# Kernel optimization log

Measured on AMD Instinct MI355X. Metric: run time of the kernel, lower is better.

## Reference

```python
import jax, jax.numpy as jnp
import numpy as np
import math

B, S, D = 8, 4096, 128  # batch, seq_len, embed_dim == attention_head_size
EPS = 1e-5


def layer_norm(x, w, b):
    mu = jnp.mean(x, axis=-1, keepdims=True)
    var = jnp.var(x, axis=-1, keepdims=True)
    return (x - mu) * jax.lax.rsqrt(var + EPS) * w + b


def setup_inputs() -> dict:
    key = jax.random.key(0)
    ks = jax.random.split(key, 4)
    x = jax.random.normal(ks[0], (B, S, D), dtype=jnp.float32)
    Wq = jax.random.normal(ks[1], (D, D), dtype=jnp.float32) / math.sqrt(D)
    Wk = jax.random.normal(ks[2], (D, D), dtype=jnp.float32) / math.sqrt(D)
    Wv = jax.random.normal(ks[3], (D, D), dtype=jnp.float32) / math.sqrt(D)
    qn_w = jnp.ones((D,), dtype=jnp.float32)
    qn_b = jnp.zeros((D,), dtype=jnp.float32)
    kn_w = jnp.ones((D,), dtype=jnp.float32)
    kn_b = jnp.zeros((D,), dtype=jnp.float32)
    return {"x": x, "Wq": Wq, "Wk": Wk, "Wv": Wv,
            "qn_w": qn_w, "qn_b": qn_b, "kn_w": kn_w, "kn_b": kn_b}


def reference(x, Wq, Wk, Wv, qn_w, qn_b, kn_w, kn_b):
    # q/k/v projections (nn.Linear with no bias: x @ W^T)
    q = layer_norm(jnp.einsum('bsd,hd->bsh', x, Wq), qn_w, qn_b)
    k = layer_norm(jnp.einsum('bsd,hd->bsh', x, Wk), kn_w, kn_b)
    v = jnp.einsum('bsd,hd->bsh', x, Wv)
    scale = math.sqrt(D)
    scores = jnp.einsum('bqh,bkh->bqk', q, k) / scale  # [B, S, S]
    attn = jax.nn.softmax(scores, axis=-1)
    # dropout_rate = 0.0 -> identity
    return jnp.einsum('bqk,bkh->bqh', attn, v)
```

## Files before the change

kernel.cpp:

```cpp
#include <hip/hip_runtime.h>

#define B_ 8
#define S_ 4096
#define D_ 128
#define KVB 64
#define NT (S_ / KVB)

typedef __attribute__((ext_vector_type(4))) float f32x4;
typedef __attribute__((ext_vector_type(16))) float f32x16;
typedef __attribute__((ext_vector_type(8))) short s16x8;

__device__ __forceinline__ unsigned short f2bf(float f) {
    union { float f; unsigned u; } v; v.f = f;
    unsigned r = (v.u + 0x7fffu + ((v.u >> 16) & 1u)) >> 16;
    return (unsigned short)r;
}

__device__ __forceinline__ unsigned cvt_pk(float lo, float hi) {
    unsigned r;
    asm("v_cvt_pk_bf16_f32 %0, %1, %2" : "=v"(r) : "v"(lo), "v"(hi));
    return r;
}

__device__ __forceinline__ s16x8 load_cvt8(const float* p) {
    f32x4 a = *(const f32x4*)p;
    f32x4 b = *(const f32x4*)(p + 4);
    s16x8 r;
    r[0] = (short)f2bf(a[0]); r[1] = (short)f2bf(a[1]);
    r[2] = (short)f2bf(a[2]); r[3] = (short)f2bf(a[3]);
    r[4] = (short)f2bf(b[0]); r[5] = (short)f2bf(b[1]);
    r[6] = (short)f2bf(b[2]); r[7] = (short)f2bf(b[3]);
    return r;
}

__device__ __forceinline__ void gld16(unsigned short* lds, const unsigned short* g) {
    __builtin_amdgcn_global_load_lds(
        (const __attribute__((address_space(1))) unsigned int*)g,
        (__attribute__((address_space(3))) unsigned int*)lds,
        16, 0, 0);
}

__global__ __launch_bounds__(256, 1) void proj_kernel(
    const float* __restrict__ x,  const float* __restrict__ Wq,
    const float* __restrict__ Wk, const float* __restrict__ Wv,
    const float* __restrict__ qn_w, const float* __restrict__ qn_b,
    const float* __restrict__ kn_w, const float* __restrict__ kn_b,
    unsigned short* __restrict__ qo, unsigned short* __restrict__ ko,
    unsigned short* __restrict__ vto)
{
    __shared__ unsigned short wlds[128 * 136];
    __shared__ unsigned short vstage[128 * 72];

    const int tid  = threadIdx.x;
    const int lane = tid & 63;
    const int wv   = tid >> 6;
    const int j    = lane & 15;
    const int g    = lane >> 4;

    const int b    = blockIdx.x >> 6;
    const int sblk = (blockIdx.x & 63) * 64;
    const int srow = sblk + wv * 16;

    const float* xrow = x + ((size_t)b * S_ + srow + j) * D_;
    s16x8 af[4];
#pragma unroll
    for (int kk = 0; kk < 4; ++kk) af[kk] = load_cvt8(xrow + kk * 32 + g * 8);

    const int wrow = tid >> 1;
    const int wcol = (tid & 1) * 64;

#pragma unroll 1
    for (int m = 0; m < 3; ++m) {
        const float* Wm = (m == 0) ? Wq : (m == 1) ? Wk : Wv;
        __syncthreads();
#pragma unroll
        for (int it = 0; it < 8; ++it) {
            int col = wcol + it * 8;
            *(s16x8*)&wlds[wrow * 136 + col] = load_cvt8(Wm + wrow * 128 + col);
        }
        __syncthreads();

        f32x4 acc[8];
#pragma unroll
        for (int ct = 0; ct < 8; ++ct) { f32x4 z = {0.f, 0.f, 0.f, 0.f}; acc[ct] = z; }
#pragma unroll
        for (int ct = 0; ct < 8; ++ct) {
#pragma unroll
            for (int kk = 0; kk < 4; ++kk) {
                s16x8 bf = *(const s16x8*)&wlds[(ct * 16 + j) * 136 + kk * 32 + g * 8];
                acc[ct] = __builtin_amdgcn_mfma_f32_16x16x32_bf16(af[kk], bf, acc[ct], 0, 0, 0);
            }
        }

        if (m < 2) {
            const float* lw = (m == 0) ? qn_w : kn_w;
            const float* lb = (m == 0) ? qn_b : kn_b;
            float sum[4], sq[4];
#pragma unroll
            for (int r = 0; r < 4; ++r) {
                float s1 = 0.f, s2 = 0.f;
#pragma unroll
                for (int ct = 0; ct < 8; ++ct) { float v = acc[ct][r]; s1 += v; s2 += v * v; }
#pragma unroll
                for (int msk = 1; msk < 16; msk <<= 1) {
                    s1 += __shfl_xor(s1, msk);
                    s2 += __shfl_xor(s2, msk);
                }
                sum[r] = s1; sq[r] = s2;
            }
            float gwv[8], gbv[8];
#pragma unroll
            for (int ct = 0; ct < 8; ++ct) { gwv[ct] = lw[ct * 16 + j]; gbv[ct] = lb[ct * 16 + j]; }
            unsigned short* dst = (m == 0) ? qo : ko;
            const float post = (m == 0) ? 0.12751742361888f : 1.0f;
#pragma unroll
            for (int r = 0; r < 4; ++r) {
                float mean = sum[r] * (1.f / 128.f);
                float var  = sq[r] * (1.f / 128.f) - mean * mean;
                float rstd = rsqrtf(var + 1e-5f);
                size_t rowoff = ((size_t)b * S_ + sblk + wv * 16 + g * 4 + r) * D_;
#pragma unroll
                for (int ct = 0; ct < 8; ++ct) {
                    float val = ((acc[ct][r] - mean) * rstd * gwv[ct] + gbv[ct]) * post;
                    dst[rowoff + ct * 16 + j] = f2bf(val);
                }
            }
        } else {
#pragma unroll
            for (int ct = 0; ct < 8; ++ct) {
#pragma unroll
                for (int r = 0; r < 4; ++r) {
                    vstage[(ct * 16 + j) * 72 + wv * 16 + g * 4 + r] = f2bf(acc[ct][r]);
                }
            }
            __syncthreads();
            int h  = tid >> 1;
            int cb = (tid & 1) * 32;
#pragma unroll
            for (int c = 0; c < 4; ++c) {
                *(s16x8*)(vto + ((size_t)b * D_ + h) * S_ + sblk + cb + c * 8) =
                    *(const s16x8*)&vstage[h * 72 + cb + c * 8];
            }
        }
    }
}

__global__ __launch_bounds__(256, 2) void attn_kernel(
    const unsigned short* __restrict__ qb, const unsigned short* __restrict__ kb,
    const unsigned short* __restrict__ vtb, float* __restrict__ out)
{
    __shared__ unsigned short kbuf[2][KVB * D_];
    __shared__ unsigned short vbuf[2][D_ * KVB];

    const int tid  = threadIdx.x;
    const int lane = tid & 63;
    const int wv   = tid >> 6;
    const int qg   = wv & 1;
    const int kh   = wv >> 1;
    const int a    = lane & 31;
    const int hh   = lane >> 5;

    const int blk = (a >> 2) & 3;
    const int pa  = (blk == 1) ? a + 4 : (blk == 2) ? a - 4 : a;

    const int swz = (blockIdx.x & 7) * 64 + (blockIdx.x >> 3);
    const int b   = swz >> 6;
    const int s0  = (swz & 63) * 64;

    const unsigned short* qptr = qb + ((size_t)b * S_ + s0 + qg * 32 + a) * D_;
    s16x8 qf[8];
#pragma unroll
    for (int kk = 0; kk < 8; ++kk) qf[kk] = *(const s16x8*)(qptr + kk * 16 + hh * 8);

    const unsigned short* kg_base = kb  + (size_t)b * S_ * D_;
    const unsigned short* vg_base = vtb + (size_t)b * D_ * S_;

    auto STAGE = [&](int bi, int kt2) {
        const int kv0 = kt2 * KVB;
#pragma unroll
        for (int it = 0; it < 4; ++it) {
            const int row = wv * 16 + it * 4 + (lane >> 4);
            const unsigned short* src =
                kg_base + (size_t)(kv0 + row) * D_ + (((lane & 15) ^ (row & 15)) << 3);
            gld16(&kbuf[bi][(wv * 16 + it * 4) * D_], src);
        }
#pragma unroll
        for (int it = 0; it < 4; ++it) {
            const int row = wv * 32 + it * 8 + (lane >> 3);
            const unsigned short* src =
                vg_base + (size_t)row * S_ + kv0 + (((lane & 7) ^ ((lane >> 3) & 7)) << 3);
            gld16(&vbuf[bi][(wv * 32 + it * 8) * KVB], src);
        }
    };

    STAGE(0, 0);
    STAGE(1, 1);

    f32x16 acc[4], ld;
#pragma unroll
    for (int dt = 0; dt < 4; ++dt)
#pragma unroll
        for (int e = 0; e < 16; ++e) acc[dt][e] = 0.f;
#pragma unroll
    for (int e = 0; e < 16; ++e) ld[e] = 0.f;

    s16x8 ones;
#pragma unroll
    for (int e = 0; e < 8; ++e) ones[e] = (short)0x3F80;

    const int kbase = (32 * kh + pa) * D_;
    const int kswz  = pa & 15;
    const int vswz  = lane & 7;

    s16x8 vfr[8];
    union PU { unsigned u[4]; s16x8 v; };
    PU P0, P1;

    auto PV_PREV = [&]() {
        __builtin_amdgcn_s_setprio(1);
        ld = __builtin_amdgcn_mfma_f32_32x32x16_bf16(P0.v, ones, ld, 0, 0, 0);
        ld = __builtin_amdgcn_mfma_f32_32x32x16_bf16(P1.v, ones, ld, 0, 0, 0);
#pragma unroll
        for (int dt = 0; dt < 4; ++dt) {
            acc[dt] = __builtin_amdgcn_mfma_f32_32x32x16_bf16(P0.v, vfr[dt * 2 + 0], acc[dt], 0, 0, 0);
            acc[dt] = __builtin_amdgcn_mfma_f32_32x32x16_bf16(P1.v, vfr[dt * 2 + 1], acc[dt], 0, 0, 0);
        }
        __builtin_amdgcn_s_setprio(0);
    };

#pragma unroll 1
    for (int kt = 0; kt < NT; ++kt) {
        const int cur = kt & 1;
        if (kt + 1 < NT) { asm volatile("s_waitcnt vmcnt(8)" ::: "memory"); }
        else             { asm volatile("s_waitcnt vmcnt(0)" ::: "memory"); }
        __builtin_amdgcn_s_barrier();
        asm volatile("" ::: "memory");

        const unsigned short* kl = kbuf[cur];
        const unsigned short* vl = vbuf[cur];

        s16x8 kf[8];
#pragma unroll
        for (int kk = 0; kk < 8; ++kk)
            kf[kk] = *(const s16x8*)&kl[kbase + (((2 * kk + hh) ^ kswz) << 3)];

        if (kt) PV_PREV();

        f32x16 sv;
#pragma unroll
        for (int e = 0; e < 16; ++e) sv[e] = 0.f;
        __builtin_amdgcn_s_setprio(1);
#pragma unroll
        for (int kk = 0; kk < 8; ++kk)
            sv = __builtin_amdgcn_mfma_f32_32x32x16_bf16(kf[kk], qf[kk], sv, 0, 0, 0);
        __builtin_amdgcn_s_setprio(0);

#pragma unroll
        for (int dt = 0; dt < 4; ++dt)
#pragma unroll
            for (int km = 0; km < 2; ++km)
                vfr[dt * 2 + km] = *(const s16x8*)
                    &vl[(32 * dt + a) * KVB + (((4 * kh + 2 * km + hh) ^ vswz) << 3)];

        float p[16];
#pragma unroll
        for (int e = 0; e < 16; ++e) p[e] = exp2f(sv[e]);
        P0.u[0] = cvt_pk(p[0],  p[1]);  P0.u[1] = cvt_pk(p[2],  p[3]);
        P0.u[2] = cvt_pk(p[4],  p[5]);  P0.u[3] = cvt_pk(p[6],  p[7]);
        P1.u[0] = cvt_pk(p[8],  p[9]);  P1.u[1] = cvt_pk(p[10], p[11]);
        P1.u[2] = cvt_pk(p[12], p[13]); P1.u[3] = cvt_pk(p[14], p[15]);

        asm volatile("s_waitcnt lgkmcnt(0)" ::: "memory");
        __builtin_amdgcn_s_barrier();
        asm volatile("" ::: "memory");
        if (kt + 2 < NT) STAGE(cur, kt + 2);
    }

    PV_PREV();

    __syncthreads();

    float* csum = (float*)&kbuf[0][0];
    float* lsum = (float*)&vbuf[0][0];
    if (kh == 1) {
#pragma unroll
        for (int dt = 0; dt < 4; ++dt)
#pragma unroll
            for (int rr = 0; rr < 4; ++rr) {
                f32x4 c4 = { acc[dt][rr*4+0], acc[dt][rr*4+1], acc[dt][rr*4+2], acc[dt][rr*4+3] };
                *(f32x4*)&csum[((qg * 4 + dt) * 4 + rr) * 256 + lane * 4] = c4;
            }
#pragma unroll
        for (int rr = 0; rr < 4; ++rr) {
            f32x4 l4 = { ld[rr*4+0], ld[rr*4+1], ld[rr*4+2], ld[rr*4+3] };
            *(f32x4*)&lsum[(qg * 4 + rr) * 256 + lane * 4] = l4;
        }
    }
    __syncthreads();
    if (kh == 0) {
        float li[16];
#pragma unroll
        for (int rr = 0; rr < 4; ++rr) {
            f32x4 lt = *(const f32x4*)&lsum[(qg * 4 + rr) * 256 + lane * 4];
#pragma unroll
            for (int e = 0; e < 4; ++e) li[rr * 4 + e] = 1.0f / (ld[rr * 4 + e] + lt[e]);
        }
#pragma unroll
        for (int dt = 0; dt < 4; ++dt) {
#pragma unroll
            for (int rr = 0; rr < 4; ++rr) {
                f32x4 o4 = *(const f32x4*)&csum[((qg * 4 + dt) * 4 + rr) * 256 + lane * 4];
#pragma unroll
                for (int e = 0; e < 4; ++e) {
                    const int r = rr * 4 + e;
                    const int qrow = (r & 3) + 8 * (r >> 2) + 4 * hh;
                    out[((size_t)b * S_ + s0 + qg * 32 + qrow) * D_ + 32 * dt + a] =
                        (acc[dt][r] + o4[e]) * li[r];
                }
            }
        }
    }
}

extern "C" void kernel_launch(void* const* d_in, const int* in_sizes, int n_in,
                              void* d_out, int out_size, void* d_ws, size_t ws_size,
                              hipStream_t stream) {
    const float* x    = (const float*)d_in[0];
    const float* Wq   = (const float*)d_in[1];
    const float* Wk   = (const float*)d_in[2];
    const float* Wv   = (const float*)d_in[3];
    const float* qn_w = (const float*)d_in[4];
    const float* qn_b = (const float*)d_in[5];
    const float* kn_w = (const float*)d_in[6];
    const float* kn_b = (const float*)d_in[7];
    float* out = (float*)d_out;

    const size_t n = (size_t)B_ * S_ * D_;
    unsigned short* qws  = (unsigned short*)d_ws;
    unsigned short* kws  = qws + n;
    unsigned short* vtws = kws + n;

    proj_kernel<<<512, 256, 0, stream>>>(x, Wq, Wk, Wv, qn_w, qn_b, kn_w, kn_b,
                                         qws, kws, vtws);
    attn_kernel<<<512, 256, 0, stream>>>(qws, kws, vtws, out);
}
```

Before: 129.3 us.

## Interleave PV MFMAs with V fragment loads and split QK accumulation chain

Restructures the attention main loop so the previous tile's PV MFMAs are split into two halves, each interleaved with reads of the V fragments for the current tile from LDS. The end-of-tile barrier and the staging of the tile two ahead are moved before the QK score MFMAs, so global prefetch is issued earlier and the score compute plus exp overlaps it. The QK dot product is split into two independent accumulators to shorten the dependent MFMA chain, at the cost of an extra vector add and more registers.

```diff
diff --git a/kernel.cpp b/kernel.cpp
--- a/kernel.cpp
+++ b/kernel.cpp
@@ -216,18 +216,6 @@
     union PU { unsigned u[4]; s16x8 v; };
     PU P0, P1;
 
-    auto PV_PREV = [&]() {
-        __builtin_amdgcn_s_setprio(1);
-        ld = __builtin_amdgcn_mfma_f32_32x32x16_bf16(P0.v, ones, ld, 0, 0, 0);
-        ld = __builtin_amdgcn_mfma_f32_32x32x16_bf16(P1.v, ones, ld, 0, 0, 0);
-#pragma unroll
-        for (int dt = 0; dt < 4; ++dt) {
-            acc[dt] = __builtin_amdgcn_mfma_f32_32x32x16_bf16(P0.v, vfr[dt * 2 + 0], acc[dt], 0, 0, 0);
-            acc[dt] = __builtin_amdgcn_mfma_f32_32x32x16_bf16(P1.v, vfr[dt * 2 + 1], acc[dt], 0, 0, 0);
-        }
-        __builtin_amdgcn_s_setprio(0);
-    };
-
 #pragma unroll 1
     for (int kt = 0; kt < NT; ++kt) {
         const int cur = kt & 1;
@@ -244,39 +232,74 @@
         for (int kk = 0; kk < 8; ++kk)
             kf[kk] = *(const s16x8*)&kl[kbase + (((2 * kk + hh) ^ kswz) << 3)];
 
-        if (kt) PV_PREV();
-
-        f32x16 sv;
-#pragma unroll
-        for (int e = 0; e < 16; ++e) sv[e] = 0.f;
-        __builtin_amdgcn_s_setprio(1);
-#pragma unroll
-        for (int kk = 0; kk < 8; ++kk)
-            sv = __builtin_amdgcn_mfma_f32_32x32x16_bf16(kf[kk], qf[kk], sv, 0, 0, 0);
-        __builtin_amdgcn_s_setprio(0);
-
-#pragma unroll
-        for (int dt = 0; dt < 4; ++dt)
+        if (kt) {
+            __builtin_amdgcn_s_setprio(1);
+            ld = __builtin_amdgcn_mfma_f32_32x32x16_bf16(P0.v, ones, ld, 0, 0, 0);
+            ld = __builtin_amdgcn_mfma_f32_32x32x16_bf16(P1.v, ones, ld, 0, 0, 0);
+            acc[0] = __builtin_amdgcn_mfma_f32_32x32x16_bf16(P0.v, vfr[0], acc[0], 0, 0, 0);
+            acc[0] = __builtin_amdgcn_mfma_f32_32x32x16_bf16(P1.v, vfr[1], acc[0], 0, 0, 0);
+            acc[1] = __builtin_amdgcn_mfma_f32_32x32x16_bf16(P0.v, vfr[2], acc[1], 0, 0, 0);
+            acc[1] = __builtin_amdgcn_mfma_f32_32x32x16_bf16(P1.v, vfr[3], acc[1], 0, 0, 0);
+            __builtin_amdgcn_s_setprio(0);
+        }
+#pragma unroll
+        for (int dt = 0; dt < 2; ++dt)
 #pragma unroll
             for (int km = 0; km < 2; ++km)
                 vfr[dt * 2 + km] = *(const s16x8*)
                     &vl[(32 * dt + a) * KVB + (((4 * kh + 2 * km + hh) ^ vswz) << 3)];
+        if (kt) {
+            __builtin_amdgcn_s_setprio(1);
+            acc[2] = __builtin_amdgcn_mfma_f32_32x32x16_bf16(P0.v, vfr[4], acc[2], 0, 0, 0);
+            acc[2] = __builtin_amdgcn_mfma_f32_32x32x16_bf16(P1.v, vfr[5], acc[2], 0, 0, 0);
+            acc[3] = __builtin_amdgcn_mfma_f32_32x32x16_bf16(P0.v, vfr[6], acc[3], 0, 0, 0);
+            acc[3] = __builtin_amdgcn_mfma_f32_32x32x16_bf16(P1.v, vfr[7], acc[3], 0, 0, 0);
+            __builtin_amdgcn_s_setprio(0);
+        }
+#pragma unroll
+        for (int dt = 2; dt < 4; ++dt)
+#pragma unroll
+            for (int km = 0; km < 2; ++km)
+                vfr[dt * 2 + km] = *(const s16x8*)
+                    &vl[(32 * dt + a) * KVB + (((4 * kh + 2 * km + hh) ^ vswz) << 3)];
+
+        asm volatile("s_waitcnt lgkmcnt(0)" ::: "memory");
+        __builtin_amdgcn_s_barrier();
+        asm volatile("" ::: "memory");
+
+        if (kt + 2 < NT) STAGE(cur, kt + 2);
+
+        f32x16 svA, svB;
+#pragma unroll
+        for (int e = 0; e < 16; ++e) { svA[e] = 0.f; svB[e] = 0.f; }
+        __builtin_amdgcn_s_setprio(1);
+#pragma unroll
+        for (int kk = 0; kk < 4; ++kk) {
+            svA = __builtin_amdgcn_mfma_f32_32x32x16_bf16(kf[kk],     qf[kk],     svA, 0, 0, 0);
+            svB = __builtin_amdgcn_mfma_f32_32x32x16_bf16(kf[kk + 4], qf[kk + 4], svB, 0, 0, 0);
+        }
+        __builtin_amdgcn_s_setprio(0);
 
         float p[16];
 #pragma unroll
-        for (int e = 0; e < 16; ++e) p[e] = exp2f(sv[e]);
+        for (int e = 0; e < 16; ++e) p[e] = exp2f(svA[e] + svB[e]);
         P0.u[0] = cvt_pk(p[0],  p[1]);  P0.u[1] = cvt_pk(p[2],  p[3]);
         P0.u[2] = cvt_pk(p[4],  p[5]);  P0.u[3] = cvt_pk(p[6],  p[7]);
         P1.u[0] = cvt_pk(p[8],  p[9]);  P1.u[1] = cvt_pk(p[10], p[11]);
         P1.u[2] = cvt_pk(p[12], p[13]); P1.u[3] = cvt_pk(p[14], p[15]);
-
-        asm volatile("s_waitcnt lgkmcnt(0)" ::: "memory");
-        __builtin_amdgcn_s_barrier();
-        asm volatile("" ::: "memory");
-        if (kt + 2 < NT) STAGE(cur, kt + 2);
-    }
-
-    PV_PREV();
+    }
+
+    {
+        __builtin_amdgcn_s_setprio(1);
+        ld = __builtin_amdgcn_mfma_f32_32x32x16_bf16(P0.v, ones, ld, 0, 0, 0);
+        ld = __builtin_amdgcn_mfma_f32_32x32x16_bf16(P1.v, ones, ld, 0, 0, 0);
+#pragma unroll
+        for (int dt = 0; dt < 4; ++dt) {
+            acc[dt] = __builtin_amdgcn_mfma_f32_32x32x16_bf16(P0.v, vfr[dt * 2 + 0], acc[dt], 0, 0, 0);
+            acc[dt] = __builtin_amdgcn_mfma_f32_32x32x16_bf16(P1.v, vfr[dt * 2 + 1], acc[dt], 0, 0, 0);
+        }
+        __builtin_amdgcn_s_setprio(0);
+    }
 
     __syncthreads();
 
```

Measured after the change: 128.2 us. No clear change (-0.8%).

## Double query rows per block and switch to triple-buffered K/V staging

Applied to the files above, without the earlier changes.

Each attention block now handles 128 query rows instead of 64, so every K/V tile staged in shared memory is reused across two 32-row query sub-tiles. The grid is halved to 256 blocks at one block per SM. K/V staging moves to a three-slot ring with a new V layout and swizzle, which removes the mid-iteration barrier and lets the next tile's loads be issued right after the QK MFMAs. The QK product is split into two independent accumulator chains that are summed before exp2 to add instruction-level parallelism. The cost is higher register pressure and lower occupancy, and with only 256 blocks the GPU may be underfilled.

```diff
diff --git a/kernel.cpp b/kernel.cpp
--- a/kernel.cpp
+++ b/kernel.cpp
@@ -145,12 +145,13 @@
     }
 }
 
-__global__ __launch_bounds__(256, 2) void attn_kernel(
+__global__ __launch_bounds__(256, 1) void attn_kernel(
     const unsigned short* __restrict__ qb, const unsigned short* __restrict__ kb,
     const unsigned short* __restrict__ vtb, float* __restrict__ out)
 {
-    __shared__ unsigned short kbuf[2][KVB * D_];
-    __shared__ unsigned short vbuf[2][D_ * KVB];
+    __shared__ unsigned short smem[49152];
+    unsigned short* kb_ = smem;
+    unsigned short* vb_ = smem + 3 * KVB * D_;
 
     const int tid  = threadIdx.x;
     const int lane = tid & 63;
@@ -163,46 +164,58 @@
     const int blk = (a >> 2) & 3;
     const int pa  = (blk == 1) ? a + 4 : (blk == 2) ? a - 4 : a;
 
-    const int swz = (blockIdx.x & 7) * 64 + (blockIdx.x >> 3);
-    const int b   = swz >> 6;
-    const int s0  = (swz & 63) * 64;
-
-    const unsigned short* qptr = qb + ((size_t)b * S_ + s0 + qg * 32 + a) * D_;
-    s16x8 qf[8];
-#pragma unroll
-    for (int kk = 0; kk < 8; ++kk) qf[kk] = *(const s16x8*)(qptr + kk * 16 + hh * 8);
+    const int swz = (blockIdx.x & 7) * 32 + (blockIdx.x >> 3);
+    const int b   = swz >> 5;
+    const int s0  = (swz & 31) * 128;
+
+    const unsigned short* qp0 = qb + ((size_t)b * S_ + s0 + qg * 64 + a) * D_;
+    const unsigned short* qp1 = qp0 + 32 * D_;
+    s16x8 qf0[8], qf1[8];
+#pragma unroll
+    for (int kk = 0; kk < 8; ++kk) {
+        qf0[kk] = *(const s16x8*)(qp0 + kk * 16 + hh * 8);
+        qf1[kk] = *(const s16x8*)(qp1 + kk * 16 + hh * 8);
+    }
 
     const unsigned short* kg_base = kb  + (size_t)b * S_ * D_;
     const unsigned short* vg_base = vtb + (size_t)b * D_ * S_;
 
     auto STAGE = [&](int bi, int kt2) {
         const int kv0 = kt2 * KVB;
+        unsigned short* kdst = kb_ + bi * (KVB * D_);
 #pragma unroll
         for (int it = 0; it < 4; ++it) {
             const int row = wv * 16 + it * 4 + (lane >> 4);
             const unsigned short* src =
                 kg_base + (size_t)(kv0 + row) * D_ + (((lane & 15) ^ (row & 15)) << 3);
-            gld16(&kbuf[bi][(wv * 16 + it * 4) * D_], src);
-        }
+            gld16(kdst + (wv * 16 + it * 4) * D_, src);
+        }
+        const int ksub = wv & 1;
+        const int rb   = 64 * (wv >> 1);
+        unsigned short* vdst = vb_ + (bi * 2 + ksub) * (D_ * 32);
 #pragma unroll
         for (int it = 0; it < 4; ++it) {
-            const int row = wv * 32 + it * 8 + (lane >> 3);
+            const int row = rb + it * 16 + (lane >> 2);
+            const int gg  = (row ^ (row >> 2)) & 3;
             const unsigned short* src =
-                vg_base + (size_t)row * S_ + kv0 + (((lane & 7) ^ ((lane >> 3) & 7)) << 3);
-            gld16(&vbuf[bi][(wv * 32 + it * 8) * KVB], src);
+                vg_base + (size_t)row * S_ + kv0 + ksub * 32 + (((lane & 3) ^ gg) << 3);
+            gld16(vdst + (rb + it * 16) * 32, src);
         }
     };
 
     STAGE(0, 0);
     STAGE(1, 1);
 
-    f32x16 acc[4], ld;
-#pragma unroll
-    for (int dt = 0; dt < 4; ++dt)
-#pragma unroll
-        for (int e = 0; e < 16; ++e) acc[dt][e] = 0.f;
-#pragma unroll
-    for (int e = 0; e < 16; ++e) ld[e] = 0.f;
+    f32x16 acc[2][4], ld[2];
+#pragma unroll
+    for (int qs = 0; qs < 2; ++qs) {
+#pragma unroll
+        for (int dt = 0; dt < 4; ++dt)
+#pragma unroll
+            for (int e = 0; e < 16; ++e) acc[qs][dt][e] = 0.f;
+#pragma unroll
+        for (int e = 0; e < 16; ++e) ld[qs][e] = 0.f;
+    }
 
     s16x8 ones;
 #pragma unroll
@@ -210,34 +223,38 @@
 
     const int kbase = (32 * kh + pa) * D_;
     const int kswz  = pa & 15;
-    const int vswz  = lane & 7;
+    const int vswz  = (a ^ (a >> 2)) & 3;
 
     s16x8 vfr[8];
     union PU { unsigned u[4]; s16x8 v; };
-    PU P0, P1;
+    PU P0a, P1a, P0b, P1b;
 
     auto PV_PREV = [&]() {
         __builtin_amdgcn_s_setprio(1);
-        ld = __builtin_amdgcn_mfma_f32_32x32x16_bf16(P0.v, ones, ld, 0, 0, 0);
-        ld = __builtin_amdgcn_mfma_f32_32x32x16_bf16(P1.v, ones, ld, 0, 0, 0);
+        ld[0] = __builtin_amdgcn_mfma_f32_32x32x16_bf16(P0a.v, ones, ld[0], 0, 0, 0);
+        ld[0] = __builtin_amdgcn_mfma_f32_32x32x16_bf16(P1a.v, ones, ld[0], 0, 0, 0);
+        ld[1] = __builtin_amdgcn_mfma_f32_32x32x16_bf16(P0b.v, ones, ld[1], 0, 0, 0);
+        ld[1] = __builtin_amdgcn_mfma_f32_32x32x16_bf16(P1b.v, ones, ld[1], 0, 0, 0);
 #pragma unroll
         for (int dt = 0; dt < 4; ++dt) {
-            acc[dt] = __builtin_amdgcn_mfma_f32_32x32x16_bf16(P0.v, vfr[dt * 2 + 0], acc[dt], 0, 0, 0);
-            acc[dt] = __builtin_amdgcn_mfma_f32_32x32x16_bf16(P1.v, vfr[dt * 2 + 1], acc[dt], 0, 0, 0);
+            acc[0][dt] = __builtin_amdgcn_mfma_f32_32x32x16_bf16(P0a.v, vfr[dt * 2 + 0], acc[0][dt], 0, 0, 0);
+            acc[0][dt] = __builtin_amdgcn_mfma_f32_32x32x16_bf16(P1a.v, vfr[dt * 2 + 1], acc[0][dt], 0, 0, 0);
+            acc[1][dt] = __builtin_amdgcn_mfma_f32_32x32x16_bf16(P0b.v, vfr[dt * 2 + 0], acc[1][dt], 0, 0, 0);
+            acc[1][dt] = __builtin_amdgcn_mfma_f32_32x32x16_bf16(P1b.v, vfr[dt * 2 + 1], acc[1][dt], 0, 0, 0);
         }
         __builtin_amdgcn_s_setprio(0);
     };
 
+    int cur = 0;
 #pragma unroll 1
     for (int kt = 0; kt < NT; ++kt) {
-        const int cur = kt & 1;
         if (kt + 1 < NT) { asm volatile("s_waitcnt vmcnt(8)" ::: "memory"); }
         else             { asm volatile("s_waitcnt vmcnt(0)" ::: "memory"); }
         __builtin_amdgcn_s_barrier();
         asm volatile("" ::: "memory");
 
-        const unsigned short* kl = kbuf[cur];
-        const unsigned short* vl = vbuf[cur];
+        const unsigned short* kl = kb_ + cur * (KVB * D_);
+        const unsigned short* vl = vb_ + (cur * 2 + kh) * (D_ * 32);
 
         s16x8 kf[8];
 #pragma unroll
@@ -246,76 +263,80 @@
 
         if (kt) PV_PREV();
 
-        f32x16 sv;
-#pragma unroll
-        for (int e = 0; e < 16; ++e) sv[e] = 0.f;
-        __builtin_amdgcn_s_setprio(1);
-#pragma unroll
-        for (int kk = 0; kk < 8; ++kk)
-            sv = __builtin_amdgcn_mfma_f32_32x32x16_bf16(kf[kk], qf[kk], sv, 0, 0, 0);
-        __builtin_amdgcn_s_setprio(0);
-
 #pragma unroll
         for (int dt = 0; dt < 4; ++dt)
 #pragma unroll
             for (int km = 0; km < 2; ++km)
                 vfr[dt * 2 + km] = *(const s16x8*)
-                    &vl[(32 * dt + a) * KVB + (((4 * kh + 2 * km + hh) ^ vswz) << 3)];
-
-        float p[16];
-#pragma unroll
-        for (int e = 0; e < 16; ++e) p[e] = exp2f(sv[e]);
-        P0.u[0] = cvt_pk(p[0],  p[1]);  P0.u[1] = cvt_pk(p[2],  p[3]);
-        P0.u[2] = cvt_pk(p[4],  p[5]);  P0.u[3] = cvt_pk(p[6],  p[7]);
-        P1.u[0] = cvt_pk(p[8],  p[9]);  P1.u[1] = cvt_pk(p[10], p[11]);
-        P1.u[2] = cvt_pk(p[12], p[13]); P1.u[3] = cvt_pk(p[14], p[15]);
-
-        asm volatile("s_waitcnt lgkmcnt(0)" ::: "memory");
-        __builtin_amdgcn_s_barrier();
-        asm volatile("" ::: "memory");
-        if (kt + 2 < NT) STAGE(cur, kt + 2);
+                    &vl[(32 * dt + a) * 32 + (((2 * km + hh) ^ vswz) << 3)];
+
+        f32x16 svA0, svB0, svA1, svB1;
+#pragma unroll
+        for (int e = 0; e < 16; ++e) { svA0[e] = 0.f; svB0[e] = 0.f; svA1[e] = 0.f; svB1[e] = 0.f; }
+        __builtin_amdgcn_s_setprio(1);
+#pragma unroll
+        for (int kk = 0; kk < 4; ++kk) {
+            svA0 = __builtin_amdgcn_mfma_f32_32x32x16_bf16(kf[kk],     qf0[kk],     svA0, 0, 0, 0);
+            svA1 = __builtin_amdgcn_mfma_f32_32x32x16_bf16(kf[kk],     qf1[kk],     svA1, 0, 0, 0);
+            svB0 = __builtin_amdgcn_mfma_f32_32x32x16_bf16(kf[kk + 4], qf0[kk + 4], svB0, 0, 0, 0);
+            svB1 = __builtin_amdgcn_mfma_f32_32x32x16_bf16(kf[kk + 4], qf1[kk + 4], svB1, 0, 0, 0);
+        }
+        __builtin_amdgcn_s_setprio(0);
+
+        if (kt + 2 < NT) {
+            int nxt = cur + 2; if (nxt >= 3) nxt -= 3;
+            STAGE(nxt, kt + 2);
+        }
+
+        float p0[16], p1[16];
+#pragma unroll
+        for (int e = 0; e < 16; ++e) {
+            p0[e] = exp2f(svA0[e] + svB0[e]);
+            p1[e] = exp2f(svA1[e] + svB1[e]);
+        }
+        P0a.u[0] = cvt_pk(p0[0],  p0[1]);  P0a.u[1] = cvt_pk(p0[2],  p0[3]);
+        P0a.u[2] = cvt_pk(p0[4],  p0[5]);  P0a.u[3] = cvt_pk(p0[6],  p0[7]);
+        P1a.u[0] = cvt_pk(p0[8],  p0[9]);  P1a.u[1] = cvt_pk(p0[10], p0[11]);
+        P1a.u[2] = cvt_pk(p0[12], p0[13]); P1a.u[3] = cvt_pk(p0[14], p0[15]);
+        P0b.u[0] = cvt_pk(p1[0],  p1[1]);  P0b.u[1] = cvt_pk(p1[2],  p1[3]);
+        P0b.u[2] = cvt_pk(p1[4],  p1[5]);  P0b.u[3] = cvt_pk(p1[6],  p1[7]);
+        P1b.u[0] = cvt_pk(p1[8],  p1[9]);  P1b.u[1] = cvt_pk(p1[10], p1[11]);
+        P1b.u[2] = cvt_pk(p1[12], p1[13]); P1b.u[3] = cvt_pk(p1[14], p1[15]);
+
+        ++cur; if (cur == 3) cur = 0;
     }
 
     PV_PREV();
 
     __syncthreads();
 
-    float* csum = (float*)&kbuf[0][0];
-    float* lsum = (float*)&vbuf[0][0];
+    float* csum = (float*)smem;
+    float* lsum = (float*)smem + 16384;
     if (kh == 1) {
 #pragma unroll
-        for (int dt = 0; dt < 4; ++dt)
-#pragma unroll
-            for (int rr = 0; rr < 4; ++rr) {
-                f32x4 c4 = { acc[dt][rr*4+0], acc[dt][rr*4+1], acc[dt][rr*4+2], acc[dt][rr*4+3] };
-                *(f32x4*)&csum[((qg * 4 + dt) * 4 + rr) * 256 + lane * 4] = c4;
-            }
-#pragma unroll
-        for (int rr = 0; rr < 4; ++rr) {
-            f32x4 l4 = { ld[rr*4+0], ld[rr*4+1], ld[rr*4+2], ld[rr*4+3] };
-            *(f32x4*)&lsum[(qg * 4 + rr) * 256 + lane * 4] = l4;
+        for (int qs = 0; qs < 2; ++qs) {
+#pragma unroll
+            for (int dt = 0; dt < 4; ++dt)
+                *(f32x16*)&csum[(((qg * 2 + qs) * 4 + dt) * 64 + lane) * 16] = acc[qs][dt];
+            *(f32x16*)&lsum[((qg * 2 + qs) * 64 + lane) * 16] = ld[qs];
         }
     }
     __syncthreads();
     if (kh == 0) {
-        float li[16];
-#pragma unroll
-        for (int rr = 0; rr < 4; ++rr) {
-            f32x4 lt = *(const f32x4*)&lsum[(qg * 4 + rr) * 256 + lane * 4];
-#pragma unroll
-            for (int e = 0; e < 4; ++e) li[rr * 4 + e] = 1.0f / (ld[rr * 4 + e] + lt[e]);
-        }
-#pragma unroll
-        for (int dt = 0; dt < 4; ++dt) {
-#pragma unroll
-            for (int rr = 0; rr < 4; ++rr) {
-                f32x4 o4 = *(const f32x4*)&csum[((qg * 4 + dt) * 4 + rr) * 256 + lane * 4];
-#pragma unroll
-                for (int e = 0; e < 4; ++e) {
-                    const int r = rr * 4 + e;
+#pragma unroll
+        for (int qs = 0; qs < 2; ++qs) {
+            f32x16 lt = *(const f32x16*)&lsum[((qg * 2 + qs) * 64 + lane) * 16];
+            float li[16];
+#pragma unroll
+            for (int r = 0; r < 16; ++r) li[r] = 1.0f / (ld[qs][r] + lt[r]);
+#pragma unroll
+            for (int dt = 0; dt < 4; ++dt) {
+                f32x16 o = *(const f32x16*)&csum[(((qg * 2 + qs) * 4 + dt) * 64 + lane) * 16];
+#pragma unroll
+                for (int r = 0; r < 16; ++r) {
                     const int qrow = (r & 3) + 8 * (r >> 2) + 4 * hh;
-                    out[((size_t)b * S_ + s0 + qg * 32 + qrow) * D_ + 32 * dt + a] =
-                        (acc[dt][r] + o4[e]) * li[r];
+                    out[((size_t)b * S_ + s0 + qg * 64 + qs * 32 + qrow) * D_ + 32 * dt + a] =
+                        (acc[qs][dt][r] + o[r]) * li[r];
                 }
             }
         }
@@ -342,5 +363,5 @@
 
     proj_kernel<<<512, 256, 0, stream>>>(x, Wq, Wk, Wv, qn_w, qn_b, kn_w, kn_b,
                                          qws, kws, vtws);
-    attn_kernel<<<512, 256, 0, stream>>>(qws, kws, vtws, out);
-}
+    attn_kernel<<<256, 256, 0, stream>>>(qws, kws, vtws, out);
+}
```

Measured after the change: 138.8 us. 7.4% more time.
